# Performance work log

Hardware: AMD Instinct MI355X
Metric: run time of the kernel (lower is better)

Reference implementation:

```python
import jax, jax.numpy as jnp
import numpy as np
from jax import lax

BN_EPS = 1e-5

@jax.custom_vjp
def ste_sign(x):
    # Binarize to {-1, +1} (sign; 0 maps to 0 like torch.sign, negligible measure)
    return jnp.sign(x)

def _ste_fwd(x):
    return jnp.sign(x), x

def _ste_bwd(x, g):
    # Straight-through estimator: pass gradient where |x| <= 1
    return (g * (jnp.abs(x) <= 1.0).astype(g.dtype),)

ste_sign.defvjp(_ste_fwd, _ste_bwd)

def bin_conv3x3(x, w, stride=1):
    # Binarize both activations and weights, then 3x3 conv, padding=1, no bias
    xb = ste_sign(x)
    wb = ste_sign(w)
    return lax.conv_general_dilated(
        xb, wb, window_strides=(stride, stride), padding=((1, 1), (1, 1)),
        dimension_numbers=('NCHW', 'OIHW', 'NCHW'))

def batchnorm_inf(x, gamma, beta, mean, var):
    # Inference-mode BatchNorm2d over channel dim (axis=1)
    scale = gamma * lax.rsqrt(var + BN_EPS)
    shift = beta - mean * scale
    return x * scale[None, :, None, None] + shift[None, :, None, None]

def hardtanh(x):
    # SelfTanh modeled as hardtanh (standard BNN activation with STE-style grad)
    return jnp.clip(x, -1.0, 1.0)

def setup_inputs() -> dict:
    key = jax.random.key(0)
    ks = jax.random.split(key, 3)
    N, C, H, W = 64, 256, 56, 56
    x = jax.random.normal(ks[0], (N, C, H, W), dtype=jnp.float32)
    w1 = jax.random.normal(ks[1], (C, C, 3, 3), dtype=jnp.float32) * (1.0 / math_sqrt(9 * C))
    w2 = jax.random.normal(ks[2], (C, C, 3, 3), dtype=jnp.float32) * (1.0 / math_sqrt(9 * C))
    ones = jnp.ones((C,), jnp.float32)
    zeros = jnp.zeros((C,), jnp.float32)
    return {
        'x': x,
        'w1': w1, 'g1': ones, 'b1': zeros, 'm1': zeros, 'v1': ones,
        'w2': w2, 'g2': ones, 'b2': zeros, 'm2': zeros, 'v2': ones,
    }

def math_sqrt(v):
    return float(np.sqrt(v))

def reference(x, w1, g1, b1, m1, v1, w2, g2, b2, m2, v2):
    residual = x
    out = bin_conv3x3(x, w1, stride=1)
    out = batchnorm_inf(out, g1, b1, m1, v1)
    out = hardtanh(out)
    out = bin_conv3x3(out, w2, stride=1)
    out = batchnorm_inf(out, g2, b2, m2, v2)
    out = out + residual
    out = hardtanh(out)
    return out
```

## Files before the change

kernel.cpp:

```cpp
#include <hip/hip_runtime.h>
#include <stdint.h>


#define NB 64
#define C  256
#define H  56
#define W  56
#define HP 58
#define PPIX 272

typedef int v4i __attribute__((ext_vector_type(4)));

__global__ __launch_bounds__(256)
void pack_x_kernel(const float* __restrict__ x, int8_t* __restrict__ Aq) {
    const int h = blockIdx.x, n = blockIdx.y;
    const int w  = threadIdx.x & 63;
    const int cg = threadIdx.x >> 6;
    if (w >= 56) return;
    const float* xp = x + (((size_t)n * C + cg * 64) * H + h) * W + w;
    uint32_t pk[16];
#pragma unroll
    for (int q = 0; q < 16; ++q) {
        uint32_t u = 0;
#pragma unroll
        for (int b = 0; b < 4; ++b) {
            float v = xp[(size_t)(q * 4 + b) * (H * W)];
            uint32_t t = (v < 0.0f) ? 0xFFu : ((v != 0.0f) ? 1u : 0u);
            u |= t << (8 * b);
        }
        pk[q] = u;
    }
    int8_t* dst = Aq + (((size_t)n * HP + h + 1) * HP + w + 1) * C + cg * 64;
#pragma unroll
    for (int q2 = 0; q2 < 4; ++q2) {
        uint4 st; st.x = pk[4*q2]; st.y = pk[4*q2+1]; st.z = pk[4*q2+2]; st.w = pk[4*q2+3];
        *(uint4*)(dst + q2 * 16) = st;
    }
}

__global__ __launch_bounds__(64)
void pack_w_kernel(const float* __restrict__ wa, const float* __restrict__ wb,
                   int8_t* __restrict__ B1, int8_t* __restrict__ B2) {
    const int kstep = blockIdx.x;
    const int nfrag = blockIdx.y;
    const float* wsrc = blockIdx.z ? wb : wa;
    int8_t* dst       = blockIdx.z ? B2 : B1;
    const int lane = threadIdx.x, quad = lane >> 4, l16 = lane & 15;
    const int co = nfrag * 16 + l16;
    uint32_t pk[4];
#pragma unroll
    for (int d = 0; d < 4; ++d) {
        uint32_t u = 0;
#pragma unroll
        for (int bb = 0; bb < 4; ++bb) {
            int k = kstep * 64 + quad * 16 + d * 4 + bb;
            int tap = k >> 8, ci = k & 255;
            float v = wsrc[((size_t)co * C + ci) * 9 + tap];
            uint32_t t = (v < 0.0f) ? 0xFFu : ((v != 0.0f) ? 1u : 0u);
            u |= t << (8 * bb);
        }
        pk[d] = u;
    }
    uint4 st; st.x = pk[0]; st.y = pk[1]; st.z = pk[2]; st.w = pk[3];
    *(uint4*)(dst + ((size_t)(nfrag * 36 + kstep) * 64 + lane) * 16) = st;
}

template <int STAGE>
__global__ __launch_bounds__(256, 2)
void mconv_kernel(const int8_t* __restrict__ Aq, const int8_t* __restrict__ Bpk,
                  const float* __restrict__ gamma, const float* __restrict__ beta,
                  const float* __restrict__ mean,  const float* __restrict__ var,
                  const float* __restrict__ resid,
                  int8_t* __restrict__ Bout, float* __restrict__ out) {
    const int h2 = blockIdx.x;
    const int n  = blockIdx.y;
    const int tid = threadIdx.x;
    const int wv = tid >> 6, lane = tid & 63, quad = lane >> 4, l16 = lane & 15;

    __shared__ int8_t lds[4 * HP * PPIX];

    const int8_t* gA = Aq + ((size_t)n * HP + h2 * 2) * HP * C;
    for (int idx = tid; idx < 4 * HP * 16; idx += 256) {
        int pix = idx >> 4, c16 = idx & 15;
        v4i val = *(const v4i*)(gA + (size_t)pix * C + c16 * 16);
        *(v4i*)(&lds[pix * PPIX + c16 * 16]) = val;
    }
    __syncthreads();

    int pixbase[7];
#pragma unroll
    for (int f = 0; f < 7; ++f) {
        int mm = f * 16 + l16;
        int hl = (mm >= 56) ? 1 : 0;
        int w  = mm - 56 * hl;
        pixbase[f] = (hl * HP + w) * PPIX + quad * 16;
    }

    const v4i* bpn[4];
#pragma unroll
    for (int nf = 0; nf < 4; ++nf)
        bpn[nf] = (const v4i*)Bpk + ((size_t)((wv * 4 + nf) * 36) * 64 + lane);

    v4i acc[7][4];
#pragma unroll
    for (int f = 0; f < 7; ++f)
#pragma unroll
        for (int nf = 0; nf < 4; ++nf)
            acc[f][nf] = (v4i){0, 0, 0, 0};

#pragma unroll 1
    for (int tap = 0; tap < 9; ++tap) {
        const int r = tap / 3, c = tap % 3;
        const int Sbase = (r * HP + c) * PPIX;
        int abase[7];
#pragma unroll
        for (int f = 0; f < 7; ++f) abase[f] = pixbase[f] + Sbase;

#pragma unroll
        for (int cich = 0; cich < 4; ++cich) {
            v4i bfr[4];
#pragma unroll
            for (int nf = 0; nf < 4; ++nf)
                bfr[nf] = bpn[nf][(size_t)tap * 256 + cich * 64];
            v4i afr[7];
#pragma unroll
            for (int f = 0; f < 7; ++f)
                afr[f] = *(const v4i*)(&lds[abase[f] + cich * 64]);
#pragma unroll
            for (int f = 0; f < 7; ++f)
#pragma unroll
                for (int nf = 0; nf < 4; ++nf)
                    acc[f][nf] = __builtin_amdgcn_mfma_i32_16x16x64_i8(
                        afr[f], bfr[nf], acc[f][nf], 0, 0, 0);
        }
    }

#pragma unroll
    for (int nf = 0; nf < 4; ++nf) {
        const int co = (wv * 4 + nf) * 16 + l16;
        double sc_d = (double)gamma[co] / sqrt((double)var[co] + 1e-5);
        float scale = (float)sc_d;
        float shift = (float)((double)beta[co] - (double)mean[co] * sc_d);
#pragma unroll
        for (int f = 0; f < 7; ++f) {
#pragma unroll
            for (int reg = 0; reg < 4; ++reg) {
                int mm = f * 16 + quad * 4 + reg;
                int hl = (mm >= 56) ? 1 : 0;
                int w  = mm - 56 * hl;
                int oh = h2 * 2 + hl;
                float v = __fadd_rn(__fmul_rn((float)acc[f][nf][reg], scale), shift);
                if (STAGE == 1) {
                    int8_t t = (v < 0.0f) ? (int8_t)-1 : ((v != 0.0f) ? (int8_t)1 : (int8_t)0);
                    Bout[(((size_t)n * HP + oh + 1) * HP + (w + 1)) * C + co] = t;
                } else {
                    size_t oidx = (((size_t)n * C + co) * H + oh) * W + w;
                    float o = v + resid[oidx];
                    o = fminf(1.0f, fmaxf(-1.0f, o));
                    out[oidx] = o;
                }
            }
        }
    }
}

extern "C" void kernel_launch(void* const* d_in, const int* in_sizes, int n_in,
                              void* d_out, int out_size, void* d_ws, size_t ws_size,
                              hipStream_t stream) {
    const float* x  = (const float*)d_in[0];
    const float* w1 = (const float*)d_in[1];
    const float* g1 = (const float*)d_in[2];
    const float* b1 = (const float*)d_in[3];
    const float* m1 = (const float*)d_in[4];
    const float* v1 = (const float*)d_in[5];
    const float* w2 = (const float*)d_in[6];
    const float* g2 = (const float*)d_in[7];
    const float* b2 = (const float*)d_in[8];
    const float* m2 = (const float*)d_in[9];
    const float* v2 = (const float*)d_in[10];
    float* out = (float*)d_out;

    uint8_t* ws = (uint8_t*)d_ws;
    const size_t ASZ = (size_t)NB * HP * HP * C;
    const size_t WPK = (size_t)16 * 36 * 64 * 16;
    int8_t* Aq   = (int8_t*)(ws);
    int8_t* Bq   = (int8_t*)(ws + ASZ);
    int8_t* Bpk1 = (int8_t*)(ws + 2 * ASZ);
    int8_t* Bpk2 = (int8_t*)(ws + 2 * ASZ + WPK);

    hipMemsetAsync(ws, 0, 2 * ASZ, stream);

    pack_w_kernel<<<dim3(36, 16, 2), 64, 0, stream>>>(w1, w2, Bpk1, Bpk2);
    pack_x_kernel<<<dim3(H, NB), 256, 0, stream>>>(x, Aq);
    mconv_kernel<1><<<dim3(28, NB), 256, 0, stream>>>(Aq, Bpk1, g1, b1, m1, v1,
                                                      nullptr, Bq, nullptr);
    mconv_kernel<2><<<dim3(28, NB), 256, 0, stream>>>(Bq, Bpk2, g2, b2, m2, v2,
                                                      x, nullptr, out);
}
```

Baseline: 666.3 us.

## Split conv blocks over output-channel halves, reuse LDS slot for fourth input row

The conv grid gains a third dimension that splits the 256 output channels into two halves. Waves within a block are split across pixel fragments (4 and 3) and channel groups. LDS shrinks from four input rows to three: after the first two kernel rows, the slot of the first input row is overwritten with the fourth. This cuts shared memory and registers per block so three blocks can fit per CU. Stage 1 output is staged through LDS for coalesced 16-byte int8 stores, stage 2 uses float4 residual loads and stores, and the full workspace memset is replaced by a kernel that zeroes only the halo borders. The cost is an extra barrier with a mid-loop reload, and the second channel-half block re-reads the same activations.

```diff
diff --git a/kernel.cpp b/kernel.cpp
--- a/kernel.cpp
+++ b/kernel.cpp
@@ -8,6 +8,8 @@
 #define W  56
 #define HP 58
 #define PPIX 272
+#define SLOT (HP * PPIX)
+#define OST 144
 
 typedef int v4i __attribute__((ext_vector_type(4)));
 
@@ -65,103 +67,194 @@
     *(uint4*)(dst + ((size_t)(nfrag * 36 + kstep) * 64 + lane) * 16) = st;
 }
 
+__global__ __launch_bounds__(256)
+void halo_zero_kernel(int8_t* __restrict__ Aq, int8_t* __restrict__ Bq) {
+    const int n = blockIdx.x;
+    int8_t* buf = blockIdx.y ? Bq : Aq;
+    const v4i z = (v4i){0, 0, 0, 0};
+    for (int idx = threadIdx.x; idx < 228 * 16; idx += 256) {
+        int px = idx >> 4, c16 = idx & 15;
+        int row, col;
+        if (px < 58)       { row = 0;  col = px; }
+        else if (px < 116) { row = 57; col = px - 58; }
+        else { int i = px - 116; row = 1 + (i >> 1); col = (i & 1) * 57; }
+        *(v4i*)(buf + (((size_t)n * HP + row) * HP + col) * C + c16 * 16) = z;
+    }
+}
+
+template <int STAGE, int NF, int F0>
+__device__ __forceinline__ void mconv_body(
+    int8_t* lds, const int8_t* __restrict__ gA, const int8_t* __restrict__ Bpk,
+    const float* __restrict__ gamma, const float* __restrict__ beta,
+    const float* __restrict__ mean,  const float* __restrict__ var,
+    const float* __restrict__ resid,
+    int8_t* __restrict__ Bout, float* __restrict__ out,
+    int n, int h2, int nb, int tid)
+{
+    const int lane = tid & 63, quad = lane >> 4, l16 = lane & 15;
+    const int ng = (tid >> 6) & 1;
+
+    int a1b[NF], a2b[NF];
+#pragma unroll
+    for (int f = 0; f < NF; ++f) {
+        int mm = (F0 + f) * 16 + l16;
+        int hl = (mm >= 56) ? 1 : 0;
+        int w  = mm - 56 * hl;
+        a1b[f] = hl * SLOT + w * PPIX + quad * 16;
+        a2b[f] = (2 - 2 * hl) * SLOT + w * PPIX + quad * 16;
+    }
+
+    const v4i* bp[4];
+#pragma unroll
+    for (int nf = 0; nf < 4; ++nf)
+        bp[nf] = (const v4i*)Bpk + ((size_t)((nb * 8 + ng * 4 + nf) * 36) * 64 + lane);
+
+    v4i acc[NF][4];
+#pragma unroll
+    for (int f = 0; f < NF; ++f)
+#pragma unroll
+        for (int nf = 0; nf < 4; ++nf) acc[f][nf] = (v4i){0, 0, 0, 0};
+
+#pragma unroll 1
+    for (int t = 0; t < 6; ++t) {
+        const int tr = (t >= 3) ? 1 : 0;
+        const int tc = t - 3 * tr;
+        const int au = tr * SLOT + tc * PPIX;
+#pragma unroll
+        for (int cich = 0; cich < 4; ++cich) {
+            v4i bfr[4];
+#pragma unroll
+            for (int nf = 0; nf < 4; ++nf)
+                bfr[nf] = bp[nf][(t * 4 + cich) * 64];
+            v4i afr[NF];
+#pragma unroll
+            for (int f = 0; f < NF; ++f)
+                afr[f] = *(const v4i*)(lds + a1b[f] + au + cich * 64);
+#pragma unroll
+            for (int f = 0; f < NF; ++f)
+#pragma unroll
+                for (int nf = 0; nf < 4; ++nf)
+                    acc[f][nf] = __builtin_amdgcn_mfma_i32_16x16x64_i8(
+                        afr[f], bfr[nf], acc[f][nf], 0, 0, 0);
+        }
+    }
+
+    __syncthreads();
+    for (int idx = tid; idx < HP * 16; idx += 256) {
+        int pix = idx >> 4, c16 = idx & 15;
+        *(v4i*)(lds + pix * PPIX + c16 * 16) =
+            *(const v4i*)(gA + ((size_t)(3 * HP + pix)) * C + c16 * 16);
+    }
+    __syncthreads();
+
+#pragma unroll 1
+    for (int t = 0; t < 3; ++t) {
+        const int au = t * PPIX;
+#pragma unroll
+        for (int cich = 0; cich < 4; ++cich) {
+            v4i bfr[4];
+#pragma unroll
+            for (int nf = 0; nf < 4; ++nf)
+                bfr[nf] = bp[nf][((6 + t) * 4 + cich) * 64];
+            v4i afr[NF];
+#pragma unroll
+            for (int f = 0; f < NF; ++f)
+                afr[f] = *(const v4i*)(lds + a2b[f] + au + cich * 64);
+#pragma unroll
+            for (int f = 0; f < NF; ++f)
+#pragma unroll
+                for (int nf = 0; nf < 4; ++nf)
+                    acc[f][nf] = __builtin_amdgcn_mfma_i32_16x16x64_i8(
+                        afr[f], bfr[nf], acc[f][nf], 0, 0, 0);
+        }
+    }
+
+    if (STAGE == 1) {
+        __syncthreads();
+#pragma unroll
+        for (int nf = 0; nf < 4; ++nf) {
+            const int co = (nb * 8 + ng * 4 + nf) * 16 + l16;
+            double scd = (double)gamma[co] / sqrt((double)var[co] + 1e-5);
+            float scale = (float)scd;
+            float shift = (float)((double)beta[co] - (double)mean[co] * scd);
+            const int col = ng * 64 + nf * 16 + l16;
+#pragma unroll
+            for (int f = 0; f < NF; ++f) {
+#pragma unroll
+                for (int reg = 0; reg < 4; ++reg) {
+                    int mm = (F0 + f) * 16 + quad * 4 + reg;
+                    float v = __fadd_rn(__fmul_rn((float)acc[f][nf][reg], scale), shift);
+                    int8_t t8 = (v < 0.0f) ? (int8_t)-1
+                              : ((v != 0.0f) ? (int8_t)1 : (int8_t)0);
+                    lds[mm * OST + col] = t8;
+                }
+            }
+        }
+        __syncthreads();
+        for (int idx = tid; idx < 112 * 8; idx += 256) {
+            int mm = idx >> 3, c = idx & 7;
+            int hl = (mm >= 56) ? 1 : 0;
+            int ww = mm - 56 * hl;
+            int oh = h2 * 2 + hl;
+            *(v4i*)(Bout + (((size_t)n * HP + oh + 1) * HP + ww + 1) * C + nb * 128 + c * 16)
+                = *(const v4i*)(lds + mm * OST + c * 16);
+        }
+    } else {
+#pragma unroll
+        for (int nf = 0; nf < 4; ++nf) {
+            const int co = (nb * 8 + ng * 4 + nf) * 16 + l16;
+            double scd = (double)gamma[co] / sqrt((double)var[co] + 1e-5);
+            float scale = (float)scd;
+            float shift = (float)((double)beta[co] - (double)mean[co] * scd);
+#pragma unroll
+            for (int f = 0; f < NF; ++f) {
+                int mmb = (F0 + f) * 16 + quad * 4;
+                int hl = (mmb >= 56) ? 1 : 0;
+                int w0 = mmb - 56 * hl;
+                int oh = h2 * 2 + hl;
+                size_t ridx = (((size_t)n * C + co) * H + oh) * W + w0;
+                float4 rv = *(const float4*)(resid + ridx);
+                float rr[4] = {rv.x, rv.y, rv.z, rv.w};
+                float oo[4];
+#pragma unroll
+                for (int reg = 0; reg < 4; ++reg) {
+                    float v = __fadd_rn(__fmul_rn((float)acc[f][nf][reg], scale), shift);
+                    float o = v + rr[reg];
+                    oo[reg] = fminf(1.0f, fmaxf(-1.0f, o));
+                }
+                float4 ov; ov.x = oo[0]; ov.y = oo[1]; ov.z = oo[2]; ov.w = oo[3];
+                *(float4*)(out + ridx) = ov;
+            }
+        }
+    }
+}
+
 template <int STAGE>
-__global__ __launch_bounds__(256, 2)
+__global__ __launch_bounds__(256, 3)
 void mconv_kernel(const int8_t* __restrict__ Aq, const int8_t* __restrict__ Bpk,
                   const float* __restrict__ gamma, const float* __restrict__ beta,
                   const float* __restrict__ mean,  const float* __restrict__ var,
                   const float* __restrict__ resid,
                   int8_t* __restrict__ Bout, float* __restrict__ out) {
-    const int h2 = blockIdx.x;
-    const int n  = blockIdx.y;
+    const int h2 = blockIdx.x, n = blockIdx.y, nb = blockIdx.z;
     const int tid = threadIdx.x;
-    const int wv = tid >> 6, lane = tid & 63, quad = lane >> 4, l16 = lane & 15;
-
-    __shared__ int8_t lds[4 * HP * PPIX];
+    __shared__ int8_t lds[3 * SLOT];
 
     const int8_t* gA = Aq + ((size_t)n * HP + h2 * 2) * HP * C;
-    for (int idx = tid; idx < 4 * HP * 16; idx += 256) {
-        int pix = idx >> 4, c16 = idx & 15;
-        v4i val = *(const v4i*)(gA + (size_t)pix * C + c16 * 16);
-        *(v4i*)(&lds[pix * PPIX + c16 * 16]) = val;
+    for (int idx = tid; idx < 3 * HP * 16; idx += 256) {
+        int d = idx / (HP * 16);
+        int pix = (idx % (HP * 16)) >> 4, c16 = idx & 15;
+        *(v4i*)(lds + d * SLOT + pix * PPIX + c16 * 16) =
+            *(const v4i*)(gA + ((size_t)(d * HP + pix)) * C + c16 * 16);
     }
     __syncthreads();
 
-    int pixbase[7];
-#pragma unroll
-    for (int f = 0; f < 7; ++f) {
-        int mm = f * 16 + l16;
-        int hl = (mm >= 56) ? 1 : 0;
-        int w  = mm - 56 * hl;
-        pixbase[f] = (hl * HP + w) * PPIX + quad * 16;
-    }
-
-    const v4i* bpn[4];
-#pragma unroll
-    for (int nf = 0; nf < 4; ++nf)
-        bpn[nf] = (const v4i*)Bpk + ((size_t)((wv * 4 + nf) * 36) * 64 + lane);
-
-    v4i acc[7][4];
-#pragma unroll
-    for (int f = 0; f < 7; ++f)
-#pragma unroll
-        for (int nf = 0; nf < 4; ++nf)
-            acc[f][nf] = (v4i){0, 0, 0, 0};
-
-#pragma unroll 1
-    for (int tap = 0; tap < 9; ++tap) {
-        const int r = tap / 3, c = tap % 3;
-        const int Sbase = (r * HP + c) * PPIX;
-        int abase[7];
-#pragma unroll
-        for (int f = 0; f < 7; ++f) abase[f] = pixbase[f] + Sbase;
-
-#pragma unroll
-        for (int cich = 0; cich < 4; ++cich) {
-            v4i bfr[4];
-#pragma unroll
-            for (int nf = 0; nf < 4; ++nf)
-                bfr[nf] = bpn[nf][(size_t)tap * 256 + cich * 64];
-            v4i afr[7];
-#pragma unroll
-            for (int f = 0; f < 7; ++f)
-                afr[f] = *(const v4i*)(&lds[abase[f] + cich * 64]);
-#pragma unroll
-            for (int f = 0; f < 7; ++f)
-#pragma unroll
-                for (int nf = 0; nf < 4; ++nf)
-                    acc[f][nf] = __builtin_amdgcn_mfma_i32_16x16x64_i8(
-                        afr[f], bfr[nf], acc[f][nf], 0, 0, 0);
-        }
-    }
-
-#pragma unroll
-    for (int nf = 0; nf < 4; ++nf) {
-        const int co = (wv * 4 + nf) * 16 + l16;
-        double sc_d = (double)gamma[co] / sqrt((double)var[co] + 1e-5);
-        float scale = (float)sc_d;
-        float shift = (float)((double)beta[co] - (double)mean[co] * sc_d);
-#pragma unroll
-        for (int f = 0; f < 7; ++f) {
-#pragma unroll
-            for (int reg = 0; reg < 4; ++reg) {
-                int mm = f * 16 + quad * 4 + reg;
-                int hl = (mm >= 56) ? 1 : 0;
-                int w  = mm - 56 * hl;
-                int oh = h2 * 2 + hl;
-                float v = __fadd_rn(__fmul_rn((float)acc[f][nf][reg], scale), shift);
-                if (STAGE == 1) {
-                    int8_t t = (v < 0.0f) ? (int8_t)-1 : ((v != 0.0f) ? (int8_t)1 : (int8_t)0);
-                    Bout[(((size_t)n * HP + oh + 1) * HP + (w + 1)) * C + co] = t;
-                } else {
-                    size_t oidx = (((size_t)n * C + co) * H + oh) * W + w;
-                    float o = v + resid[oidx];
-                    o = fminf(1.0f, fmaxf(-1.0f, o));
-                    out[oidx] = o;
-                }
-            }
-        }
-    }
+    if ((tid >> 7) == 0)
+        mconv_body<STAGE, 4, 0>(lds, gA, Bpk, gamma, beta, mean, var, resid,
+                                Bout, out, n, h2, nb, tid);
+    else
+        mconv_body<STAGE, 3, 4>(lds, gA, Bpk, gamma, beta, mean, var, resid,
+                                Bout, out, n, h2, nb, tid);
 }
 
 extern "C" void kernel_launch(void* const* d_in, const int* in_sizes, int n_in,
@@ -188,12 +281,11 @@
     int8_t* Bpk1 = (int8_t*)(ws + 2 * ASZ);
     int8_t* Bpk2 = (int8_t*)(ws + 2 * ASZ + WPK);
 
-    hipMemsetAsync(ws, 0, 2 * ASZ, stream);
-
+    halo_zero_kernel<<<dim3(NB, 2), 256, 0, stream>>>(Aq, Bq);
     pack_w_kernel<<<dim3(36, 16, 2), 64, 0, stream>>>(w1, w2, Bpk1, Bpk2);
     pack_x_kernel<<<dim3(H, NB), 256, 0, stream>>>(x, Aq);
-    mconv_kernel<1><<<dim3(28, NB), 256, 0, stream>>>(Aq, Bpk1, g1, b1, m1, v1,
-                                                      nullptr, Bq, nullptr);
-    mconv_kernel<2><<<dim3(28, NB), 256, 0, stream>>>(Bq, Bpk2, g2, b2, m2, v2,
-                                                      x, nullptr, out);
-}
+    mconv_kernel<1><<<dim3(28, NB, 2), 256, 0, stream>>>(Aq, Bpk1, g1, b1, m1, v1,
+                                                         nullptr, Bq, nullptr);
+    mconv_kernel<2><<<dim3(28, NB, 2), 256, 0, stream>>>(Bq, Bpk2, g2, b2, m2, v2,
+                                                         x, nullptr, out);
+}
```

After: 697.2 us. 1.05x slower.

## Zero only halos, stage outputs through LDS, prefetch weights, vectorize epilogue

Applied to the files above, without the earlier changes.

Replaces the full-workspace memset with a kernel that zeroes only the padding halo of the two padded activation buffers. The stage-1 epilogue is restaged through LDS so the sign bytes go to global memory as coalesced 16-byte stores instead of scattered single bytes, and pack_x does the same. The stage-2 epilogue reads the residual and writes the output with float4 accesses, BN scale and shift are precomputed once by a small kernel, and the weight fragments are register double-buffered one K-step ahead. This adds extra launches and LDS round-trips, and the weight prefetch reads slightly past the last fragment block into adjacent workspace.

```diff
diff --git a/kernel.cpp b/kernel.cpp
--- a/kernel.cpp
+++ b/kernel.cpp
@@ -8,6 +8,8 @@
 #define W  56
 #define HP 58
 #define PPIX 272
+#define SLOT (HP * PPIX)
+#define OST 272
 
 typedef int v4i __attribute__((ext_vector_type(4)));
 
@@ -15,26 +17,29 @@
 void pack_x_kernel(const float* __restrict__ x, int8_t* __restrict__ Aq) {
     const int h = blockIdx.x, n = blockIdx.y;
     const int w  = threadIdx.x & 63;
-    const int cg = threadIdx.x >> 6;
-    if (w >= 56) return;
-    const float* xp = x + (((size_t)n * C + cg * 64) * H + h) * W + w;
-    uint32_t pk[16];
-#pragma unroll
-    for (int q = 0; q < 16; ++q) {
+    const int cq = threadIdx.x >> 6;
+
+    __shared__ int8_t st[56 * OST];
+
+    const float* xp = x + (((size_t)n * C + cq * 64) * H + h) * W + w;
+#pragma unroll
+    for (int i = 0; i < 16; ++i) {
         uint32_t u = 0;
 #pragma unroll
         for (int b = 0; b < 4; ++b) {
-            float v = xp[(size_t)(q * 4 + b) * (H * W)];
+            float v = (w < 56) ? xp[(size_t)(i * 4 + b) * (H * W)] : 0.0f;
             uint32_t t = (v < 0.0f) ? 0xFFu : ((v != 0.0f) ? 1u : 0u);
             u |= t << (8 * b);
         }
-        pk[q] = u;
-    }
-    int8_t* dst = Aq + (((size_t)n * HP + h + 1) * HP + w + 1) * C + cg * 64;
-#pragma unroll
-    for (int q2 = 0; q2 < 4; ++q2) {
-        uint4 st; st.x = pk[4*q2]; st.y = pk[4*q2+1]; st.z = pk[4*q2+2]; st.w = pk[4*q2+3];
-        *(uint4*)(dst + q2 * 16) = st;
+        if (w < 56)
+            *(uint32_t*)(st + w * OST + cq * 64 + i * 4) = u;
+    }
+    __syncthreads();
+    int8_t* dst = Aq + (((size_t)n * HP + h + 1) * HP + 1) * C;
+    for (int idx = threadIdx.x; idx < 56 * 16; idx += 256) {
+        int pix = idx >> 4, c16 = idx & 15;
+        *(v4i*)(dst + (size_t)pix * C + c16 * 16) =
+            *(const v4i*)(st + pix * OST + c16 * 16);
     }
 }
 
@@ -65,11 +70,39 @@
     *(uint4*)(dst + ((size_t)(nfrag * 36 + kstep) * 64 + lane) * 16) = st;
 }
 
+__global__ __launch_bounds__(256)
+void halo_zero_kernel(int8_t* __restrict__ Aq, int8_t* __restrict__ Bq) {
+    const int n = blockIdx.x;
+    int8_t* buf = blockIdx.y ? Bq : Aq;
+    const v4i z = (v4i){0, 0, 0, 0};
+    for (int idx = threadIdx.x; idx < 228 * 16; idx += 256) {
+        int px = idx >> 4, c16 = idx & 15;
+        int row, col;
+        if (px < 58)       { row = 0;  col = px; }
+        else if (px < 116) { row = 57; col = px - 58; }
+        else { int i = px - 116; row = 1 + (i >> 1); col = (i & 1) * 57; }
+        *(v4i*)(buf + (((size_t)n * HP + row) * HP + col) * C + c16 * 16) = z;
+    }
+}
+
+__global__ __launch_bounds__(256)
+void bn_prep_kernel(const float* g1, const float* b1, const float* m1, const float* v1,
+                    const float* g2, const float* b2, const float* m2, const float* v2,
+                    float* __restrict__ sc, float* __restrict__ sh) {
+    const int co = threadIdx.x;
+    const float* g = blockIdx.x ? g2 : g1;
+    const float* b = blockIdx.x ? b2 : b1;
+    const float* m = blockIdx.x ? m2 : m1;
+    const float* v = blockIdx.x ? v2 : v1;
+    double scd = (double)g[co] / sqrt((double)v[co] + 1e-5);
+    sc[blockIdx.x * C + co] = (float)scd;
+    sh[blockIdx.x * C + co] = (float)((double)b[co] - (double)m[co] * scd);
+}
+
 template <int STAGE>
 __global__ __launch_bounds__(256, 2)
 void mconv_kernel(const int8_t* __restrict__ Aq, const int8_t* __restrict__ Bpk,
-                  const float* __restrict__ gamma, const float* __restrict__ beta,
-                  const float* __restrict__ mean,  const float* __restrict__ var,
+                  const float* __restrict__ scp, const float* __restrict__ shp,
                   const float* __restrict__ resid,
                   int8_t* __restrict__ Bout, float* __restrict__ out) {
     const int h2 = blockIdx.x;
@@ -77,88 +110,118 @@
     const int tid = threadIdx.x;
     const int wv = tid >> 6, lane = tid & 63, quad = lane >> 4, l16 = lane & 15;
 
-    __shared__ int8_t lds[4 * HP * PPIX];
+    __shared__ int8_t lds[4 * SLOT];
 
     const int8_t* gA = Aq + ((size_t)n * HP + h2 * 2) * HP * C;
     for (int idx = tid; idx < 4 * HP * 16; idx += 256) {
         int pix = idx >> 4, c16 = idx & 15;
-        v4i val = *(const v4i*)(gA + (size_t)pix * C + c16 * 16);
-        *(v4i*)(&lds[pix * PPIX + c16 * 16]) = val;
+        *(v4i*)(lds + pix * PPIX + c16 * 16) =
+            *(const v4i*)(gA + (size_t)pix * C + c16 * 16);
     }
     __syncthreads();
 
-    int pixbase[7];
+    int abase[7];
 #pragma unroll
     for (int f = 0; f < 7; ++f) {
         int mm = f * 16 + l16;
         int hl = (mm >= 56) ? 1 : 0;
         int w  = mm - 56 * hl;
-        pixbase[f] = (hl * HP + w) * PPIX + quad * 16;
-    }
-
-    const v4i* bpn[4];
+        abase[f] = hl * SLOT + w * PPIX + quad * 16;
+    }
+
+    const int8_t* bq[4];
 #pragma unroll
     for (int nf = 0; nf < 4; ++nf)
-        bpn[nf] = (const v4i*)Bpk + ((size_t)((wv * 4 + nf) * 36) * 64 + lane);
+        bq[nf] = Bpk + (size_t)((wv * 4 + nf) * 36) * 1024 + lane * 16;
+
+    v4i bcur[4];
+#pragma unroll
+    for (int nf = 0; nf < 4; ++nf) bcur[nf] = *(const v4i*)(bq[nf]);
 
     v4i acc[7][4];
 #pragma unroll
     for (int f = 0; f < 7; ++f)
 #pragma unroll
-        for (int nf = 0; nf < 4; ++nf)
-            acc[f][nf] = (v4i){0, 0, 0, 0};
+        for (int nf = 0; nf < 4; ++nf) acc[f][nf] = (v4i){0, 0, 0, 0};
 
 #pragma unroll 1
-    for (int tap = 0; tap < 9; ++tap) {
-        const int r = tap / 3, c = tap % 3;
-        const int Sbase = (r * HP + c) * PPIX;
-        int abase[7];
-#pragma unroll
-        for (int f = 0; f < 7; ++f) abase[f] = pixbase[f] + Sbase;
-
-#pragma unroll
-        for (int cich = 0; cich < 4; ++cich) {
-            v4i bfr[4];
+    for (int t = 0; t < 9; ++t) {
+        const int r = (t >= 6) ? 2 : ((t >= 3) ? 1 : 0);
+        const int c = t - 3 * r;
+        const int au = r * SLOT + c * PPIX;
+#pragma unroll
+        for (int ci = 0; ci < 4; ++ci) {
+            v4i bnxt[4];
 #pragma unroll
             for (int nf = 0; nf < 4; ++nf)
-                bfr[nf] = bpn[nf][(size_t)tap * 256 + cich * 64];
+                bnxt[nf] = *(const v4i*)(bq[nf] + (ci + 1) * 1024);
             v4i afr[7];
 #pragma unroll
             for (int f = 0; f < 7; ++f)
-                afr[f] = *(const v4i*)(&lds[abase[f] + cich * 64]);
+                afr[f] = *(const v4i*)(lds + abase[f] + au + ci * 64);
 #pragma unroll
             for (int f = 0; f < 7; ++f)
 #pragma unroll
                 for (int nf = 0; nf < 4; ++nf)
                     acc[f][nf] = __builtin_amdgcn_mfma_i32_16x16x64_i8(
-                        afr[f], bfr[nf], acc[f][nf], 0, 0, 0);
-        }
-    }
-
-#pragma unroll
-    for (int nf = 0; nf < 4; ++nf) {
-        const int co = (wv * 4 + nf) * 16 + l16;
-        double sc_d = (double)gamma[co] / sqrt((double)var[co] + 1e-5);
-        float scale = (float)sc_d;
-        float shift = (float)((double)beta[co] - (double)mean[co] * sc_d);
-#pragma unroll
-        for (int f = 0; f < 7; ++f) {
-#pragma unroll
-            for (int reg = 0; reg < 4; ++reg) {
-                int mm = f * 16 + quad * 4 + reg;
-                int hl = (mm >= 56) ? 1 : 0;
-                int w  = mm - 56 * hl;
+                        afr[f], bcur[nf], acc[f][nf], 0, 0, 0);
+#pragma unroll
+            for (int nf = 0; nf < 4; ++nf) bcur[nf] = bnxt[nf];
+        }
+#pragma unroll
+        for (int nf = 0; nf < 4; ++nf) bq[nf] += 4096;
+    }
+
+    if (STAGE == 1) {
+        __syncthreads();
+#pragma unroll
+        for (int nf = 0; nf < 4; ++nf) {
+            const int co = (wv * 4 + nf) * 16 + l16;
+            const float scale = scp[co], shift = shp[co];
+#pragma unroll
+            for (int f = 0; f < 7; ++f) {
+#pragma unroll
+                for (int reg = 0; reg < 4; ++reg) {
+                    int mm = f * 16 + quad * 4 + reg;
+                    float v = __fadd_rn(__fmul_rn((float)acc[f][nf][reg], scale), shift);
+                    int8_t t8 = (v < 0.0f) ? (int8_t)-1
+                              : ((v != 0.0f) ? (int8_t)1 : (int8_t)0);
+                    lds[mm * OST + co] = t8;
+                }
+            }
+        }
+        __syncthreads();
+        for (int idx = tid; idx < 112 * 16; idx += 256) {
+            int mm = idx >> 4, c16 = idx & 15;
+            int hl = (mm >= 56) ? 1 : 0;
+            int ww = mm - 56 * hl;
+            int oh = h2 * 2 + hl;
+            *(v4i*)(Bout + (((size_t)n * HP + oh + 1) * HP + ww + 1) * C + c16 * 16)
+                = *(const v4i*)(lds + mm * OST + c16 * 16);
+        }
+    } else {
+#pragma unroll
+        for (int nf = 0; nf < 4; ++nf) {
+            const int co = (wv * 4 + nf) * 16 + l16;
+            const float scale = scp[co], shift = shp[co];
+#pragma unroll
+            for (int f = 0; f < 7; ++f) {
+                int mmb = f * 16 + quad * 4;
+                int hl = (mmb >= 56) ? 1 : 0;
+                int w0 = mmb - 56 * hl;
                 int oh = h2 * 2 + hl;
-                float v = __fadd_rn(__fmul_rn((float)acc[f][nf][reg], scale), shift);
-                if (STAGE == 1) {
-                    int8_t t = (v < 0.0f) ? (int8_t)-1 : ((v != 0.0f) ? (int8_t)1 : (int8_t)0);
-                    Bout[(((size_t)n * HP + oh + 1) * HP + (w + 1)) * C + co] = t;
-                } else {
-                    size_t oidx = (((size_t)n * C + co) * H + oh) * W + w;
-                    float o = v + resid[oidx];
-                    o = fminf(1.0f, fmaxf(-1.0f, o));
-                    out[oidx] = o;
+                size_t ridx = (((size_t)n * C + co) * H + oh) * W + w0;
+                float4 rv = *(const float4*)(resid + ridx);
+                float rr[4] = {rv.x, rv.y, rv.z, rv.w};
+                float oo[4];
+#pragma unroll
+                for (int reg = 0; reg < 4; ++reg) {
+                    float v = __fadd_rn(__fmul_rn((float)acc[f][nf][reg], scale), shift);
+                    float o = v + rr[reg];
+                    oo[reg] = fminf(1.0f, fmaxf(-1.0f, o));
                 }
+                float4 ov; ov.x = oo[0]; ov.y = oo[1]; ov.z = oo[2]; ov.w = oo[3];
+                *(float4*)(out + ridx) = ov;
             }
         }
     }
@@ -187,13 +250,16 @@
     int8_t* Bq   = (int8_t*)(ws + ASZ);
     int8_t* Bpk1 = (int8_t*)(ws + 2 * ASZ);
     int8_t* Bpk2 = (int8_t*)(ws + 2 * ASZ + WPK);
-
-    hipMemsetAsync(ws, 0, 2 * ASZ, stream);
-
+    float*  scb  = (float*)(ws + 2 * ASZ + 2 * WPK);
+    float*  shb  = (float*)(ws + 2 * ASZ + 2 * WPK + 2048);
+
+    halo_zero_kernel<<<dim3(NB, 2), 256, 0, stream>>>(Aq, Bq);
+    bn_prep_kernel<<<dim3(2), 256, 0, stream>>>(g1, b1, m1, v1, g2, b2, m2, v2,
+                                                scb, shb);
     pack_w_kernel<<<dim3(36, 16, 2), 64, 0, stream>>>(w1, w2, Bpk1, Bpk2);
     pack_x_kernel<<<dim3(H, NB), 256, 0, stream>>>(x, Aq);
-    mconv_kernel<1><<<dim3(28, NB), 256, 0, stream>>>(Aq, Bpk1, g1, b1, m1, v1,
+    mconv_kernel<1><<<dim3(28, NB), 256, 0, stream>>>(Aq, Bpk1, scb, shb,
                                                       nullptr, Bq, nullptr);
-    mconv_kernel<2><<<dim3(28, NB), 256, 0, stream>>>(Bq, Bpk2, g2, b2, m2, v2,
+    mconv_kernel<2><<<dim3(28, NB), 256, 0, stream>>>(Bq, Bpk2, scb + C, shb + C,
                                                       x, nullptr, out);
 }
```

Result: faster. 646.1 us (-3.0%).
